# Kernel optimization log

Hardware: AMD Instinct MI355X
Metric: run time of the kernel (lower is better)

Reference implementation:

```python
import jax, jax.numpy as jnp
import numpy as np
from jax import lax

INPUT_DIM = 512
KERNEL_DIM = 3
HEADS = 8
B, L = 16, 1024


def setup_inputs() -> dict:
    key = jax.random.key(0)
    ks = jax.random.split(key, 4)
    fan = INPUT_DIM * KERNEL_DIM
    std = float(np.sqrt(2.0 / (INPUT_DIM + fan)))  # xavier_normal for conv weight
    x = jax.random.normal(ks[0], (B, INPUT_DIM, L), dtype=jnp.float32)
    w0 = jax.random.normal(ks[1], (INPUT_DIM, INPUT_DIM, KERNEL_DIM), dtype=jnp.float32) * std
    w1 = jax.random.normal(ks[2], (INPUT_DIM, INPUT_DIM, KERNEL_DIM), dtype=jnp.float32) * std
    w2 = jax.random.normal(ks[3], (INPUT_DIM, INPUT_DIM, KERNEL_DIM), dtype=jnp.float32) * std
    b0 = jnp.zeros((INPUT_DIM,), jnp.float32)
    b1 = jnp.zeros((INPUT_DIM,), jnp.float32)
    b2 = jnp.zeros((INPUT_DIM,), jnp.float32)
    return {"x": x, "w0": w0, "b0": b0, "w1": w1, "b1": b1, "w2": w2, "b2": b2}


def _conv1d(x, w, b):
    # x: [B, C, L], w: [O, I, K] -> [B, O, L-K+1] (VALID, stride 1)
    y = lax.conv_general_dilated(x, w, window_strides=(1,), padding='VALID',
                                 dimension_numbers=('NCH', 'OIH', 'NCH'))
    return y + b[None, :, None]


def _multihead_attention(q, k, v, input_dim, heads):
    # q,k,v: [B, D, Lp]; chunk along channel dim == reshape to [B, H, Dh, Lp]
    b, d, lp = q.shape
    dh = d // heads
    qh = q.reshape(b, heads, dh, lp)
    kh = k.reshape(b, heads, dh, lp)
    vh = v.reshape(b, heads, dh, lp)
    scale = 1.0 / np.sqrt(input_dim)  # NOTE: original scales by sqrt(full input_dim)
    scores = jnp.einsum('bhdq,bhdk->bhqk', qh, kh) * scale  # [B,H,Lp,Lp]
    attn = jax.nn.softmax(scores, axis=-1)
    out = jnp.einsum('bhqk,bhdk->bhdq', attn, vh)  # [B,H,Dh,Lp]
    return out.reshape(b, d, lp)


def reference(x, w0, b0, w1, b1, w2, b2):
    q = _conv1d(x, w0, b0)
    k = _conv1d(x, w1, b1)
    v = _conv1d(x, w2, b2)
    return _multihead_attention(q, k, v, INPUT_DIM, HEADS)
```

## Files before the change

### kernel.cpp

```cpp
#include <hip/hip_runtime.h>

#define B_SZ 16
#define CIN  512
#define LIN  1024
#define LP   1022
#define HEADS 8
#define DH    64

typedef __attribute__((ext_vector_type(8))) short bf16x8;
typedef __attribute__((ext_vector_type(4))) float f32x4;

__device__ inline unsigned short f2bf(float f) {
    union { float f; unsigned int u; } c; c.f = f;
    unsigned int r = c.u + 0x7FFF + ((c.u >> 16) & 1);
    return (unsigned short)(r >> 16);
}

__device__ __forceinline__ void gl_lds16(const unsigned short* g, unsigned short* l) {
    __builtin_amdgcn_global_load_lds((const __attribute__((address_space(1))) void*)g,
                                     (__attribute__((address_space(3))) void*)l, 16, 0, 0);
}

#define SWZ(G) ((G) ^ (((G) >> 3) & 7))

__global__ __launch_bounds__(256) void xb_cvt_kernel(const float* __restrict__ x,
                                                     unsigned short* __restrict__ xb) {
    __shared__ float sm[64][68];
    const int t  = threadIdx.x;
    const int l0 = blockIdx.x * 64;
    const int i0 = blockIdx.y * 64;
    const int b  = blockIdx.z;
    const float* S = x + ((size_t)b * CIN + i0) * LIN;

    #pragma unroll
    for (int rr = 0; rr < 4; rr++) {
        int idx = rr * 1024 + t * 4;
        int ii = idx >> 6, lj = idx & 63;
        *(float4*)&sm[ii][lj] = *(const float4*)(S + (size_t)ii * LIN + l0 + lj);
    }
    __syncthreads();

    #pragma unroll
    for (int rr = 0; rr < 4; rr++) {
        int idx = rr * 1024 + t * 4;
        int l = idx >> 6, dj = idx & 63;
        ushort4 h;
        h.x = f2bf(sm[dj + 0][l]);
        h.y = f2bf(sm[dj + 1][l]);
        h.z = f2bf(sm[dj + 2][l]);
        h.w = f2bf(sm[dj + 3][l]);
        *(ushort4*)(xb + ((size_t)b * 1024 + l0 + l) * 512 + i0 + dj) = h;
    }
}

__global__ __launch_bounds__(256) void wb_cvt_kernel(const float* __restrict__ w0,
                                                     const float* __restrict__ w1,
                                                     const float* __restrict__ w2,
                                                     unsigned short* __restrict__ wb) {
    const int kk = blockIdx.y;
    int flat = blockIdx.x * 256 + threadIdx.x;
    int i  = flat & 511;
    int oG = flat >> 9;
    int c  = oG >> 9, o = oG & 511;
    const float* w = (c == 0) ? w0 : (c == 1) ? w1 : w2;
    wb[(size_t)kk * 786432 + flat] = f2bf(w[o * 1536 + i * 3 + kk]);
}

__global__ __launch_bounds__(256) void conv_mfma_kernel(
        const unsigned short* __restrict__ xb,
        const unsigned short* __restrict__ wb,
        const float* __restrict__ b0, const float* __restrict__ b1,
        const float* __restrict__ b2,
        unsigned short* __restrict__ Qt, unsigned short* __restrict__ Kt,
        unsigned short* __restrict__ Vt, float qscale) {
    __shared__ unsigned short smem[16896];
    unsigned short* xs = smem;
    unsigned short* ws = smem + 4224;

    const int t    = threadIdx.x;
    const int wave = t >> 6;
    const int lane = t & 63;
    const int col  = lane & 15;
    const int quad = lane >> 4;
    const int wh   = wave >> 1;
    const int wn   = wave & 1;
    const int l0   = blockIdx.x * 128;
    const int o0   = blockIdx.y * 128;
    const int b    = blockIdx.z;

    f32x4 acc[4][4];
    #pragma unroll
    for (int i = 0; i < 4; i++)
        #pragma unroll
        for (int j = 0; j < 4; j++) acc[i][j] = (f32x4){0.f, 0.f, 0.f, 0.f};

    const unsigned short* xrow = xb + (size_t)b * 1024 * 512;

    for (int ic = 0; ic < 512; ic += 32) {
        __syncthreads();

        #pragma unroll
        for (int j = 0; j < 6; j++) {
            int instr = wave * 6 + j;
            int Gg = SWZ(instr * 64 + lane);
            int p = Gg >> 2, q = Gg & 3;
            int kk = p >> 7, orow = p & 127;
            gl_lds16(wb + ((size_t)(kk * 1536 + o0 + orow)) * 512 + ic + q * 8,
                     ws + instr * 512);
        }
        #pragma unroll
        for (int j = 0; j < 2; j++) {
            int instr = wave * 2 + j;
            int Gg = SWZ(instr * 64 + lane);
            int p = Gg >> 2, q = Gg & 3;
            gl_lds16(xrow + (size_t)(l0 + p) * 512 + ic + q * 8,
                     xs + instr * 512);
        }
        if (t < 8) {
            int row = 128 + (t >> 2), sg = t & 3;
            int gl = l0 + row;
            bf16x8 v = (bf16x8){0, 0, 0, 0, 0, 0, 0, 0};
            if (gl < 1024) v = *(const bf16x8*)(xrow + (size_t)gl * 512 + ic + sg * 8);
            *(bf16x8*)&xs[SWZ(512 + t) * 8] = v;
        }
        __syncthreads();

        #pragma unroll
        for (int kk = 0; kk < 3; kk++) {
            bf16x8 af[4], bfr[4];
            #pragma unroll
            for (int ms = 0; ms < 4; ms++) {
                int G = ((kk * 128 + wh * 64 + ms * 16 + col) << 2) | quad;
                af[ms] = *(const bf16x8*)&ws[SWZ(G) * 8];
            }
            #pragma unroll
            for (int ns = 0; ns < 4; ns++) {
                int G = ((wn * 64 + ns * 16 + col + kk) << 2) | quad;
                bfr[ns] = *(const bf16x8*)&xs[SWZ(G) * 8];
            }
            #pragma unroll
            for (int ms = 0; ms < 4; ms++)
                #pragma unroll
                for (int ns = 0; ns < 4; ns++)
                    acc[ms][ns] = __builtin_amdgcn_mfma_f32_16x16x32_bf16(af[ms], bfr[ns], acc[ms][ns], 0, 0, 0);
        }
    }

    const int c = blockIdx.y >> 2;

    if (c < 2) {
        unsigned short* dst = (c == 0) ? Qt : Kt;
        const float* bias   = (c == 0) ? b0 : b1;
        const float sc      = (c == 0) ? qscale : 1.0f;
        const int h = (((o0 & 511) + wh * 64) >> 6) & 7;
        unsigned short* base = dst + (size_t)(b * 8 + h) * 65536;
        #pragma unroll
        for (int ms = 0; ms < 4; ms++) {
            int ob = (o0 & 511) + wh * 64 + ms * 16 + quad * 4;
            float bv[4];
            #pragma unroll
            for (int r = 0; r < 4; r++) bv[r] = bias[ob + r];
            int d0 = ms * 16 + quad * 4;
            #pragma unroll
            for (int ns = 0; ns < 4; ns++) {
                int l = l0 + wn * 64 + ns * 16 + col;
                ushort4 hv;
                hv.x = f2bf((acc[ms][ns][0] + bv[0]) * sc);
                hv.y = f2bf((acc[ms][ns][1] + bv[1]) * sc);
                hv.z = f2bf((acc[ms][ns][2] + bv[2]) * sc);
                hv.w = f2bf((acc[ms][ns][3] + bv[3]) * sc);
                *(ushort4*)(base + (size_t)l * 64 + d0) = hv;
            }
        }
    } else {
        __syncthreads();
        unsigned short* vt = smem;
        #pragma unroll
        for (int ms = 0; ms < 4; ms++) {
            int ob = (o0 & 511) + wh * 64 + ms * 16 + quad * 4;
            #pragma unroll
            for (int ns = 0; ns < 4; ns++) {
                int lc = wn * 64 + ns * 16 + col;
                #pragma unroll
                for (int r = 0; r < 4; r++)
                    vt[(wh * 64 + ms * 16 + quad * 4 + r) * 132 + lc] =
                        f2bf(acc[ms][ns][r] + b2[ob + r]);
            }
        }
        __syncthreads();
        #pragma unroll
        for (int it = 0; it < 8; it++) {
            int flat = it * 2048 + t * 8;
            int row = flat >> 7, colx = flat & 127;
            bf16x8 v = *(const bf16x8*)&vt[row * 132 + colx];
            int og = (o0 & 511) + row;
            int h = og >> 6, d = og & 63;
            *(bf16x8*)(Vt + ((size_t)(b * 8 + h) * 64 + d) * 1024 + l0 + colx) = v;
        }
    }
}

__global__ __launch_bounds__(256) void attn_kernel(const unsigned short* __restrict__ Qt,
                                                   const unsigned short* __restrict__ Kt,
                                                   const unsigned short* __restrict__ Vt,
                                                   float* __restrict__ out) {
    __shared__ unsigned short smem[12800];
    unsigned short* Ks = smem;
    unsigned short* Vs = smem + 4096;
    unsigned short* Ps = smem + 8192;

    const int t    = threadIdx.x;
    const int wave = t >> 6;
    const int lane = t & 63;
    const int col  = lane & 15;
    const int quad = lane >> 4;
    const int qb   = blockIdx.x;
    const int bh   = blockIdx.y;

    const size_t base64 = (size_t)bh * 1024 * 64;
    const int q0w = qb * 64 + wave * 16;

    const unsigned short* qrow = Qt + base64 + (size_t)(q0w + col) * 64;
    bf16x8 aq0 = *(const bf16x8*)(qrow + quad * 8);
    bf16x8 aq1 = *(const bf16x8*)(qrow + 32 + quad * 8);

    const bf16x8 ones = (bf16x8){0x3F80, 0x3F80, 0x3F80, 0x3F80,
                                 0x3F80, 0x3F80, 0x3F80, 0x3F80};

    f32x4 o[4];
    #pragma unroll
    for (int d = 0; d < 4; d++) o[d] = (f32x4){0.f, 0.f, 0.f, 0.f};
    f32x4 osum = (f32x4){0.f, 0.f, 0.f, 0.f};

    const unsigned short* kg0 = Kt + base64;
    const unsigned short* vg  = Vt + base64;
    unsigned short* Pw = Ps + wave * 16 * 72;

    for (int kt = 0; kt < 16; kt++) {
        __syncthreads();

        const unsigned short* kg = kg0 + (size_t)kt * 4096;
        #pragma unroll
        for (int j = 0; j < 2; j++) {
            int i = wave + j * 4;
            int G = SWZ(i * 64 + lane);
            gl_lds16(kg + (size_t)G * 8, Ks + i * 512);
            int p = G >> 3, q = G & 7;
            gl_lds16(vg + (size_t)p * 1024 + kt * 64 + q * 8, Vs + i * 512);
        }
        __syncthreads();

        f32x4 s[4];
        #pragma unroll
        for (int sub = 0; sub < 4; sub++) {
            int row = sub * 16 + col;
            bf16x8 b0 = *(const bf16x8*)&Ks[SWZ(row * 8 + quad) * 8];
            bf16x8 b1 = *(const bf16x8*)&Ks[SWZ(row * 8 + 4 + quad) * 8];
            f32x4 a = (f32x4){0.f, 0.f, 0.f, 0.f};
            a = __builtin_amdgcn_mfma_f32_16x16x32_bf16(aq0, b0, a, 0, 0, 0);
            a = __builtin_amdgcn_mfma_f32_16x16x32_bf16(aq1, b1, a, 0, 0, 0);
            s[sub] = a;
        }

        float p[4][4];
        #pragma unroll
        for (int sub = 0; sub < 4; sub++)
            #pragma unroll
            for (int r = 0; r < 4; r++)
                p[sub][r] = exp2f(s[sub][r]);
        if (kt == 15 && col >= 14) {
            #pragma unroll
            for (int r = 0; r < 4; r++) p[3][r] = 0.f;
        }
        #pragma unroll
        for (int sub = 0; sub < 4; sub++)
            #pragma unroll
            for (int r = 0; r < 4; r++) {
                union { float f; unsigned int u; } c; c.f = p[sub][r];
                Pw[(quad * 4 + r) * 72 + sub * 16 + col] = (unsigned short)(c.u >> 16);
            }

        bf16x8 ap0 = *(const bf16x8*)&Pw[col * 72 + quad * 8];
        bf16x8 ap1 = *(const bf16x8*)&Pw[col * 72 + 32 + quad * 8];

        #pragma unroll
        for (int dsub = 0; dsub < 4; dsub++) {
            int row = dsub * 16 + col;
            bf16x8 b0 = *(const bf16x8*)&Vs[SWZ(row * 8 + quad) * 8];
            bf16x8 b1 = *(const bf16x8*)&Vs[SWZ(row * 8 + 4 + quad) * 8];
            o[dsub] = __builtin_amdgcn_mfma_f32_16x16x32_bf16(ap0, b0, o[dsub], 0, 0, 0);
            o[dsub] = __builtin_amdgcn_mfma_f32_16x16x32_bf16(ap1, b1, o[dsub], 0, 0, 0);
        }
        osum = __builtin_amdgcn_mfma_f32_16x16x32_bf16(ap0, ones, osum, 0, 0, 0);
        osum = __builtin_amdgcn_mfma_f32_16x16x32_bf16(ap1, ones, osum, 0, 0, 0);
    }

    #pragma unroll
    for (int dsub = 0; dsub < 4; dsub++) {
        int d = dsub * 16 + col;
        #pragma unroll
        for (int r = 0; r < 4; r++) {
            int q = q0w + quad * 4 + r;
            if (q < LP)
                out[((size_t)bh * 64 + d) * LP + q] = o[dsub][r] / osum[r];
        }
    }
}

extern "C" void kernel_launch(void* const* d_in, const int* in_sizes, int n_in,
                              void* d_out, int out_size, void* d_ws, size_t ws_size,
                              hipStream_t stream) {
    const float* x  = (const float*)d_in[0];
    const float* w0 = (const float*)d_in[1];
    const float* b0 = (const float*)d_in[2];
    const float* w1 = (const float*)d_in[3];
    const float* b1 = (const float*)d_in[4];
    const float* w2 = (const float*)d_in[5];
    const float* b2 = (const float*)d_in[6];
    float* out = (float*)d_out;

    unsigned short* xbp = (unsigned short*)d_ws;
    unsigned short* wbp = xbp + 8388608;
    unsigned short* Qt  = wbp + 2359296;
    unsigned short* Kt  = Qt + 8388608;
    unsigned short* Vt  = Kt + 8388608;

    const float scale = 0.06375870864f;

    xb_cvt_kernel<<<dim3(16, 8, 16), 256, 0, stream>>>(x, xbp);
    wb_cvt_kernel<<<dim3(3072, 3), 256, 0, stream>>>(w0, w1, w2, wbp);
    conv_mfma_kernel<<<dim3(8, 12, 16), 256, 0, stream>>>(xbp, wbp, b0, b1, b2,
                                                          Qt, Kt, Vt, scale);
    attn_kernel<<<dim3(16, 128), 256, 0, stream>>>(Qt, Kt, Vt, out);
}
```

Before: 261.0 us.

## Process two query tiles per wave in attention to reuse K/V fragments

Each attention wave now handles 32 queries instead of 16, so every K/V tile loaded into LDS and every K/V register fragment is reused across two query groups, and the grid is halved. The MFMA operands are swapped so scores come out transposed, which lets P be written to LDS as packed 64-bit stores and the output be stored with query index along lanes. Launch bounds are raised to 4 blocks per CU and LDS grows for the larger P buffer. Register pressure goes up and the grid has fewer blocks.

Result: faster. 241.8 us (-7.4%).

```diff
diff --git a/kernel.cpp b/kernel.cpp
--- a/kernel.cpp
+++ b/kernel.cpp
@@ -200,11 +200,12 @@
     }
 }
 
-__global__ __launch_bounds__(256) void attn_kernel(const unsigned short* __restrict__ Qt,
-                                                   const unsigned short* __restrict__ Kt,
-                                                   const unsigned short* __restrict__ Vt,
-                                                   float* __restrict__ out) {
-    __shared__ unsigned short smem[12800];
+__global__ __launch_bounds__(256, 4) void attn_kernel(
+        const unsigned short* __restrict__ Qt,
+        const unsigned short* __restrict__ Kt,
+        const unsigned short* __restrict__ Vt,
+        float* __restrict__ out) {
+    __shared__ unsigned short smem[17408];
     unsigned short* Ks = smem;
     unsigned short* Vs = smem + 4096;
     unsigned short* Ps = smem + 8192;
@@ -218,23 +219,31 @@
     const int bh   = blockIdx.y;
 
     const size_t base64 = (size_t)bh * 1024 * 64;
-    const int q0w = qb * 64 + wave * 16;
-
-    const unsigned short* qrow = Qt + base64 + (size_t)(q0w + col) * 64;
-    bf16x8 aq0 = *(const bf16x8*)(qrow + quad * 8);
-    bf16x8 aq1 = *(const bf16x8*)(qrow + 32 + quad * 8);
+    const int q0w = qb * 128 + wave * 32;
+
+    bf16x8 bq[2][2];
+    #pragma unroll
+    for (int g = 0; g < 2; g++) {
+        const unsigned short* qrow = Qt + base64 + (size_t)(q0w + g * 16 + col) * 64;
+        bq[g][0] = *(const bf16x8*)(qrow + quad * 8);
+        bq[g][1] = *(const bf16x8*)(qrow + 32 + quad * 8);
+    }
 
     const bf16x8 ones = (bf16x8){0x3F80, 0x3F80, 0x3F80, 0x3F80,
                                  0x3F80, 0x3F80, 0x3F80, 0x3F80};
 
-    f32x4 o[4];
-    #pragma unroll
-    for (int d = 0; d < 4; d++) o[d] = (f32x4){0.f, 0.f, 0.f, 0.f};
-    f32x4 osum = (f32x4){0.f, 0.f, 0.f, 0.f};
+    f32x4 o[2][4];
+    #pragma unroll
+    for (int g = 0; g < 2; g++)
+        #pragma unroll
+        for (int d = 0; d < 4; d++) o[g][d] = (f32x4){0.f, 0.f, 0.f, 0.f};
+    f32x4 osum[2];
+    osum[0] = (f32x4){0.f, 0.f, 0.f, 0.f};
+    osum[1] = (f32x4){0.f, 0.f, 0.f, 0.f};
 
     const unsigned short* kg0 = Kt + base64;
     const unsigned short* vg  = Vt + base64;
-    unsigned short* Pw = Ps + wave * 16 * 72;
+    unsigned short* Pw = Ps + wave * 32 * 72;
 
     for (int kt = 0; kt < 16; kt++) {
         __syncthreads();
@@ -250,59 +259,73 @@
         }
         __syncthreads();
 
-        f32x4 s[4];
+        bf16x8 ak[4][2];
         #pragma unroll
         for (int sub = 0; sub < 4; sub++) {
-            int row = sub * 16 + col;
-            bf16x8 b0 = *(const bf16x8*)&Ks[SWZ(row * 8 + quad) * 8];
-            bf16x8 b1 = *(const bf16x8*)&Ks[SWZ(row * 8 + 4 + quad) * 8];
-            f32x4 a = (f32x4){0.f, 0.f, 0.f, 0.f};
-            a = __builtin_amdgcn_mfma_f32_16x16x32_bf16(aq0, b0, a, 0, 0, 0);
-            a = __builtin_amdgcn_mfma_f32_16x16x32_bf16(aq1, b1, a, 0, 0, 0);
-            s[sub] = a;
-        }
-
-        float p[4][4];
-        #pragma unroll
-        for (int sub = 0; sub < 4; sub++)
-            #pragma unroll
-            for (int r = 0; r < 4; r++)
-                p[sub][r] = exp2f(s[sub][r]);
-        if (kt == 15 && col >= 14) {
-            #pragma unroll
-            for (int r = 0; r < 4; r++) p[3][r] = 0.f;
-        }
-        #pragma unroll
-        for (int sub = 0; sub < 4; sub++)
-            #pragma unroll
-            for (int r = 0; r < 4; r++) {
-                union { float f; unsigned int u; } c; c.f = p[sub][r];
-                Pw[(quad * 4 + r) * 72 + sub * 16 + col] = (unsigned short)(c.u >> 16);
-            }
-
-        bf16x8 ap0 = *(const bf16x8*)&Pw[col * 72 + quad * 8];
-        bf16x8 ap1 = *(const bf16x8*)&Pw[col * 72 + 32 + quad * 8];
-
+            int rk = sub * 16 + col;
+            ak[sub][0] = *(const bf16x8*)&Ks[SWZ(rk * 8 + quad) * 8];
+            ak[sub][1] = *(const bf16x8*)&Ks[SWZ(rk * 8 + 4 + quad) * 8];
+        }
+
+        #pragma unroll
+        for (int g = 0; g < 2; g++) {
+            #pragma unroll
+            for (int sub = 0; sub < 4; sub++) {
+                f32x4 a = (f32x4){0.f, 0.f, 0.f, 0.f};
+                a = __builtin_amdgcn_mfma_f32_16x16x32_bf16(ak[sub][0], bq[g][0], a, 0, 0, 0);
+                a = __builtin_amdgcn_mfma_f32_16x16x32_bf16(ak[sub][1], bq[g][1], a, 0, 0, 0);
+                unsigned int u[4];
+                #pragma unroll
+                for (int r = 0; r < 4; r++) {
+                    union { float f; unsigned int u; } c;
+                    c.f = exp2f(a[r]);
+                    u[r] = c.u;
+                }
+                if (kt == 15 && sub == 3 && quad == 3) {
+                    u[2] = 0; u[3] = 0;
+                }
+                uint2 pk;
+                pk.x = (u[0] >> 16) | (u[1] & 0xFFFF0000u);
+                pk.y = (u[2] >> 16) | (u[3] & 0xFFFF0000u);
+                *(uint2*)&Pw[(g * 16 + col) * 72 + sub * 16 + quad * 4] = pk;
+            }
+        }
+
+        bf16x8 av[4][2];
         #pragma unroll
         for (int dsub = 0; dsub < 4; dsub++) {
-            int row = dsub * 16 + col;
-            bf16x8 b0 = *(const bf16x8*)&Vs[SWZ(row * 8 + quad) * 8];
-            bf16x8 b1 = *(const bf16x8*)&Vs[SWZ(row * 8 + 4 + quad) * 8];
-            o[dsub] = __builtin_amdgcn_mfma_f32_16x16x32_bf16(ap0, b0, o[dsub], 0, 0, 0);
-            o[dsub] = __builtin_amdgcn_mfma_f32_16x16x32_bf16(ap1, b1, o[dsub], 0, 0, 0);
-        }
-        osum = __builtin_amdgcn_mfma_f32_16x16x32_bf16(ap0, ones, osum, 0, 0, 0);
-        osum = __builtin_amdgcn_mfma_f32_16x16x32_bf16(ap1, ones, osum, 0, 0, 0);
-    }
-
-    #pragma unroll
-    for (int dsub = 0; dsub < 4; dsub++) {
-        int d = dsub * 16 + col;
-        #pragma unroll
-        for (int r = 0; r < 4; r++) {
-            int q = q0w + quad * 4 + r;
-            if (q < LP)
-                out[((size_t)bh * 64 + d) * LP + q] = o[dsub][r] / osum[r];
+            int rd = dsub * 16 + col;
+            av[dsub][0] = *(const bf16x8*)&Vs[SWZ(rd * 8 + quad) * 8];
+            av[dsub][1] = *(const bf16x8*)&Vs[SWZ(rd * 8 + 4 + quad) * 8];
+        }
+
+        #pragma unroll
+        for (int g = 0; g < 2; g++) {
+            bf16x8 bp0 = *(const bf16x8*)&Pw[(g * 16 + col) * 72 + quad * 8];
+            bf16x8 bp1 = *(const bf16x8*)&Pw[(g * 16 + col) * 72 + 32 + quad * 8];
+            #pragma unroll
+            for (int dsub = 0; dsub < 4; dsub++) {
+                o[g][dsub] = __builtin_amdgcn_mfma_f32_16x16x32_bf16(av[dsub][0], bp0, o[g][dsub], 0, 0, 0);
+                o[g][dsub] = __builtin_amdgcn_mfma_f32_16x16x32_bf16(av[dsub][1], bp1, o[g][dsub], 0, 0, 0);
+            }
+            osum[g] = __builtin_amdgcn_mfma_f32_16x16x32_bf16(ones, bp0, osum[g], 0, 0, 0);
+            osum[g] = __builtin_amdgcn_mfma_f32_16x16x32_bf16(ones, bp1, osum[g], 0, 0, 0);
+        }
+    }
+
+    #pragma unroll
+    for (int g = 0; g < 2; g++) {
+        int q = q0w + g * 16 + col;
+        if (q < LP) {
+            float inv = 1.0f / osum[g][0];
+            #pragma unroll
+            for (int dsub = 0; dsub < 4; dsub++) {
+                #pragma unroll
+                for (int r = 0; r < 4; r++) {
+                    int d = dsub * 16 + quad * 4 + r;
+                    out[((size_t)bh * 64 + d) * LP + q] = o[g][dsub][r] * inv;
+                }
+            }
         }
     }
 }
@@ -331,5 +354,5 @@
     wb_cvt_kernel<<<dim3(3072, 3), 256, 0, stream>>>(w0, w1, w2, wbp);
     conv_mfma_kernel<<<dim3(8, 12, 16), 256, 0, stream>>>(xbp, wbp, b0, b1, b2,
                                                           Qt, Kt, Vt, scale);
-    attn_kernel<<<dim3(16, 128), 256, 0, stream>>>(Qt, Kt, Vt, out);
-}
+    attn_kernel<<<dim3(8, 128), 256, 0, stream>>>(Qt, Kt, Vt, out);
+}
```
